# Performance work log

Measured on AMD Instinct MI355X. Metric: run time of the kernel, lower is better.

## Reference

```python
import jax, jax.numpy as jnp
import numpy as np
import math

T = 0.01      # temperature (init kwarg)
CUT = 32      # high-frequency cutoff (init kwarg)


def scalar_field(n, F):
    """Random scalar field of size [n,n] from the first m=F.shape[0] sine modes."""
    m = F.shape[0]
    xs = jnp.linspace(0.0, 1.0, n, dtype=F.dtype)
    k = jnp.arange(1, m + 1, dtype=F.dtype)
    i, j = jnp.meshgrid(k, k, indexing='ij')          # [m,m]
    r = jnp.sqrt(i * i + j * j)
    e = (r < m + 0.5).astype(F.dtype) / r             # sqrt(1/energy) mask
    s = jnp.sin(math.pi * xs[:, None] * k[None, :])   # [n,m]
    c = F * e
    return jnp.einsum('ij,xi,yj->yx', c, s, s)        # [n,n]


def remap_linear(a, dx, dy):
    """Bilinear remap of a [..., n, m] by displacement fields dx, dy of shape [n,m]."""
    n, m = a.shape[-2], a.shape[-1]
    dt = dx.dtype
    yy, xx = jnp.meshgrid(jnp.arange(n, dtype=dt), jnp.arange(m, dtype=dt), indexing='ij')
    xn = jnp.clip(xx + dx, 0, m - 1)
    yn = jnp.clip(yy + dy, 0, n - 1)
    xf = jnp.floor(xn).astype(jnp.int32)
    yf = jnp.floor(yn).astype(jnp.int32)
    xc = jnp.ceil(xn).astype(jnp.int32)
    yc = jnp.ceil(yn).astype(jnp.int32)
    xv = (xn - xf.astype(dt))[None, None]  # [1,1,n,m] broadcast over batch, channel
    yv = (yn - yf.astype(dt))[None, None]
    g = lambda yi, xi: a[..., yi, xi]      # gather corners -> [B,C,n,m]
    return ((1 - yv) * (1 - xv) * g(yf, xf)
            + (1 - yv) * xv * g(yf, xc)
            + yv * (1 - xv) * g(yc, xf)
            + yv * xv * g(yc, xc))


def setup_inputs() -> dict:
    key = jax.random.key(0)
    k1, k2, k3 = jax.random.split(key, 3)
    x = jax.random.normal(k1, (128, 3, 224, 224), dtype=jnp.float32)
    F_x = jax.random.normal(k2, (CUT, CUT), dtype=jnp.float32)
    F_y = jax.random.normal(k3, (CUT, CUT), dtype=jnp.float32)
    return {"x": x, "F_x": F_x, "F_y": F_y}


def reference(x, F_x, F_y):
    n = x.shape[-1]
    u = scalar_field(n, F_x)
    v = scalar_field(n, F_y)
    dx = (T ** 0.5) * u * n
    dy = (T ** 0.5) * v * n
    return remap_linear(x, dx, dy)
```

## Files before the change

kernel.cpp:

```cpp
#include <hip/hip_runtime.h>
#include <hip/hip_fp16.h>

#define N 224
#define M 32
#define NPIX (N * N)
#define NPLANE 384
#define PLT 128
#define NPGRP 3
#define TTILE 4704
#define NPT 6
#define RPX 64
#define NCHUNK (NPIX / RPX)
#define NXCD 8
#define CPX (NCHUNK / NXCD)
#define PI_F 3.14159265358979323846f

typedef float vfloat4 __attribute__((ext_vector_type(4)));
typedef float vfloat2 __attribute__((ext_vector_type(2)));

__global__ __launch_bounds__(256) void fused_field_transpose(
    const float* __restrict__ x, const float* __restrict__ Fx,
    const float* __restrict__ Fy, int4* __restrict__ tab,
    __half* __restrict__ xt)
{
    const int tid = threadIdx.x;

    if (blockIdx.x < N) {
        __shared__ float cx[M][M];
        __shared__ float cy[M][M];
        __shared__ float sy[M];

        const int y = blockIdx.x;

        for (int idx = tid; idx < M * M; idx += 256) {
            const int i = idx / M, j = idx % M;
            const float fi = (float)(i + 1), fj = (float)(j + 1);
            const float r = sqrtf(fi * fi + fj * fj);
            const float e = (r < (float)M + 0.5f) ? (1.0f / r) : 0.0f;
            cx[i][j] = Fx[idx] * e;
            cy[i][j] = Fy[idx] * e;
        }
        if (tid < M) {
            const float ys = (float)y / (float)(N - 1);
            sy[tid] = sinf(PI_F * ys * (float)(tid + 1));
        }
        __syncthreads();

        if (tid >= N) return;
        const int xi = tid;

        float sx[M];
        const float xsv = (float)xi / (float)(N - 1);
#pragma unroll
        for (int i = 0; i < M; ++i)
            sx[i] = sinf(PI_F * xsv * (float)(i + 1));

        float u = 0.0f, v = 0.0f;
#pragma unroll 1
        for (int j = 0; j < M; ++j) {
            float tx = 0.0f, ty = 0.0f;
#pragma unroll
            for (int i = 0; i < M; ++i) {
                tx = fmaf(cx[i][j], sx[i], tx);
                ty = fmaf(cy[i][j], sx[i], ty);
            }
            const float syj = sy[j];
            u = fmaf(syj, tx, u);
            v = fmaf(syj, ty, v);
        }

        const float dxv = 22.4f * u;
        const float dyv = 22.4f * v;
        const float xn = fminf(fmaxf((float)xi + dxv, 0.0f), (float)(N - 1));
        const float yn = fminf(fmaxf((float)y + dyv, 0.0f), (float)(N - 1));
        const int bx = min((int)floorf(xn), N - 2);
        const int by = min((int)floorf(yn), N - 2);
        const float fx = xn - (float)bx;
        const float fy = yn - (float)by;

        tab[y * N + xi] = make_int4(by * N + bx,
                                    __float_as_int(fx), __float_as_int(fy), 0);
        return;
    }

    __shared__ float t[64][65];

    const int tb    = blockIdx.x - N;
    const int ptile = tb % NPT;
    const int xtile = tb / NPT;
    const int pl0   = ptile * 64;
    const int pix0  = xtile * 64;

    const int c = tid & 15;
    const int q = (tid >> 4) & 3;
    const int w = tid >> 6;

#pragma unroll
    for (int i = 0; i < 4; ++i) {
        const int p = w * 16 + i * 4 + q;
        const vfloat4 v = *(const vfloat4*)(
            x + (size_t)(pl0 + p) * NPIX + pix0 + 4 * c);
        t[p][4 * c + 0] = v.x;
        t[p][4 * c + 1] = v.y;
        t[p][4 * c + 2] = v.z;
        t[p][4 * c + 3] = v.w;
    }
    __syncthreads();

    __half* xo = xt + (size_t)pix0 * NPLANE + pl0;
#pragma unroll
    for (int s = 0; s < 4; ++s) {
        const int P = w * 16 + s * 4 + q;
        const float f0 = t[4 * c + 0][P];
        const float f1 = t[4 * c + 1][P];
        const float f2 = t[4 * c + 2][P];
        const float f3 = t[4 * c + 3][P];
        union { uint2 u; __half2 hh[2]; } pk;
        pk.hh[0] = __floats2half2_rn(f0, f1);
        pk.hh[1] = __floats2half2_rn(f2, f3);
        *(uint2*)&xo[(size_t)P * NPLANE + 4 * c] = pk.u;
    }
}

__global__ __launch_bounds__(256) void remap_kernel(
    const __half* __restrict__ xt, const int4* __restrict__ tab,
    float* __restrict__ out)
{
    __shared__ float tile[RPX][130];
    __shared__ int4 ltab[RPX];

    const int tid = threadIdx.x;
    const int w = tid >> 6, l = tid & 63;

    const int bid   = blockIdx.x;
    const int xcd   = bid & 7;
    const int local = bid >> 3;
    const int pg    = local / CPX;
    const int chunk = xcd * CPX + (local % CPX);
    const int pix0  = chunk * RPX;

    if (tid < RPX) ltab[tid] = tab[pix0 + tid];
    __syncthreads();

    const __half2* base = (const __half2*)xt;
    const int pgoff = pg * (PLT / 2);

#pragma unroll 8
    for (int i = 0; i < 16; ++i) {
        const int pl = w * 16 + i;
        const int4 tb = ltab[pl];
        const float fx = __int_as_float(tb.y);
        const float fy = __int_as_float(tb.z);
        const float omx = 1.0f - fx, omy = 1.0f - fy;
        const float w00 = omy * omx, w01 = omy * fx;
        const float w10 = fy * omx,  w11 = fy * fx;

        const size_t b0 = (size_t)tb.x * (NPLANE / 2) + pgoff;
        const float2 c00 = __half22float2(base[b0 + l]);
        const float2 c01 = __half22float2(base[b0 + NPLANE / 2 + l]);
        const float2 c10 = __half22float2(base[b0 + (size_t)N * (NPLANE/2) + l]);
        const float2 c11 = __half22float2(base[b0 + (size_t)(N + 1) * (NPLANE/2) + l]);

        float2 o;
        o.x = w00 * c00.x + w01 * c01.x + w10 * c10.x + w11 * c11.x;
        o.y = w00 * c00.y + w01 * c01.y + w10 * c10.y + w11 * c11.y;
        *(float2*)&tile[pl][2 * l] = o;
    }
    __syncthreads();

    const int l2 = tid & 31, jg = tid >> 5;
    float* ob = out + (size_t)pg * PLT * NPIX + pix0;
#pragma unroll
    for (int s = 0; s < 16; ++s) {
        const int j = jg * 16 + s;
        vfloat2 o2;
        o2.x = tile[2 * l2][j];
        o2.y = tile[2 * l2 + 1][j];
        __builtin_nontemporal_store(o2, (vfloat2*)&ob[(size_t)j * NPIX + 2 * l2]);
    }
}

extern "C" void kernel_launch(void* const* d_in, const int* in_sizes, int n_in,
                              void* d_out, int out_size, void* d_ws, size_t ws_size,
                              hipStream_t stream) {
    const float* x  = (const float*)d_in[0];
    const float* Fx = (const float*)d_in[1];
    const float* Fy = (const float*)d_in[2];
    float* out = (float*)d_out;

    int4* tab = (int4*)d_ws;
    const size_t tab_bytes = (size_t)NPIX * sizeof(int4);
    __half* xt = (__half*)((char*)d_ws + tab_bytes);

    fused_field_transpose<<<N + TTILE, 256, 0, stream>>>(x, Fx, Fy, tab, xt);
    remap_kernel<<<NCHUNK * NPGRP, 256, 0, stream>>>(xt, tab, out);
}
```

Before: 49.59 us.

## Widen transpose tiles to 128 planes with 16-byte half stores and permuted layout

Each transpose block now handles 128 planes by 64 pixels instead of 64 by 64, so there are half as many blocks, and each thread writes 16-byte packed half stores instead of 8-byte ones. The planes are interleaved in a permuted order within each 8-half group, and the remap kernel's shared-tile write index is permuted to match when it unpacks. The field-computation blocks move to the end of the grid and share one pooled shared-memory buffer. The larger shared buffer may reduce occupancy, and correctness depends on the two kernels agreeing on the permuted plane order.

```diff
diff --git a/kernel.cpp b/kernel.cpp
--- a/kernel.cpp
+++ b/kernel.cpp
@@ -7,8 +7,8 @@
 #define NPLANE 384
 #define PLT 128
 #define NPGRP 3
-#define TTILE 4704
-#define NPT 6
+#define NXT 784
+#define TTILE (NXT * NPGRP)
 #define RPX 64
 #define NCHUNK (NPIX / RPX)
 #define NXCD 8
@@ -23,14 +23,15 @@
     const float* __restrict__ Fy, int4* __restrict__ tab,
     __half* __restrict__ xt)
 {
+    __shared__ float pool[128 * 65];
     const int tid = threadIdx.x;
 
-    if (blockIdx.x < N) {
-        __shared__ float cx[M][M];
-        __shared__ float cy[M][M];
-        __shared__ float sy[M];
+    if (blockIdx.x >= TTILE) {
+        float (*cx)[M] = (float(*)[M])pool;
+        float (*cy)[M] = (float(*)[M])(pool + M * M);
+        float *sy = pool + 2 * M * M;
 
-        const int y = blockIdx.x;
+        const int y = blockIdx.x - TTILE;
 
         for (int idx = tid; idx < M * M; idx += 256) {
             const int i = idx / M, j = idx % M;
@@ -83,12 +84,12 @@
         return;
     }
 
-    __shared__ float t[64][65];
+    float (*t)[65] = (float(*)[65])pool;
 
-    const int tb    = blockIdx.x - N;
-    const int ptile = tb % NPT;
-    const int xtile = tb / NPT;
-    const int pl0   = ptile * 64;
+    const int tb    = blockIdx.x;
+    const int pg    = tb / NXT;
+    const int xtile = tb % NXT;
+    const int pl0   = pg * 128;
     const int pix0  = xtile * 64;
 
     const int c = tid & 15;
@@ -96,8 +97,8 @@
     const int w = tid >> 6;
 
 #pragma unroll
-    for (int i = 0; i < 4; ++i) {
-        const int p = w * 16 + i * 4 + q;
+    for (int i = 0; i < 8; ++i) {
+        const int p = 16 * i + (tid >> 4);
         const vfloat4 v = *(const vfloat4*)(
             x + (size_t)(pl0 + p) * NPIX + pix0 + 4 * c);
         t[p][4 * c + 0] = v.x;
@@ -111,14 +112,12 @@
 #pragma unroll
     for (int s = 0; s < 4; ++s) {
         const int P = w * 16 + s * 4 + q;
-        const float f0 = t[4 * c + 0][P];
-        const float f1 = t[4 * c + 1][P];
-        const float f2 = t[4 * c + 2][P];
-        const float f3 = t[4 * c + 3][P];
-        union { uint2 u; __half2 hh[2]; } pk;
-        pk.hh[0] = __floats2half2_rn(f0, f1);
-        pk.hh[1] = __floats2half2_rn(f2, f3);
-        *(uint2*)&xo[(size_t)P * NPLANE + 4 * c] = pk.u;
+        union { uint4 u; __half2 hh[4]; } pk;
+        pk.hh[0] = __floats2half2_rn(t[4 * c + 0][P],  t[4 * c + 1][P]);
+        pk.hh[1] = __floats2half2_rn(t[4 * c + 2][P],  t[4 * c + 3][P]);
+        pk.hh[2] = __floats2half2_rn(t[4 * c + 64][P], t[4 * c + 65][P]);
+        pk.hh[3] = __floats2half2_rn(t[4 * c + 66][P], t[4 * c + 67][P]);
+        *(uint4*)&xo[(size_t)P * NPLANE + 8 * c] = pk.u;
     }
 }
 
@@ -145,6 +144,8 @@
     const __half2* base = (const __half2*)xt;
     const int pgoff = pg * (PLT / 2);
 
+    const int r0 = 4 * (l >> 2) + 2 * (l & 1) + 64 * ((l & 3) >> 1);
+
 #pragma unroll 8
     for (int i = 0; i < 16; ++i) {
         const int pl = w * 16 + i;
@@ -164,7 +165,7 @@
         float2 o;
         o.x = w00 * c00.x + w01 * c01.x + w10 * c10.x + w11 * c11.x;
         o.y = w00 * c00.y + w01 * c01.y + w10 * c10.y + w11 * c11.y;
-        *(float2*)&tile[pl][2 * l] = o;
+        *(float2*)&tile[pl][r0] = o;
     }
     __syncthreads();
 
@@ -192,6 +193,6 @@
     const size_t tab_bytes = (size_t)NPIX * sizeof(int4);
     __half* xt = (__half*)((char*)d_ws + tab_bytes);
 
-    fused_field_transpose<<<N + TTILE, 256, 0, stream>>>(x, Fx, Fy, tab, xt);
+    fused_field_transpose<<<TTILE + N, 256, 0, stream>>>(x, Fx, Fy, tab, xt);
     remap_kernel<<<NCHUNK * NPGRP, 256, 0, stream>>>(xt, tab, out);
 }
```

New measurement: 65.55 us. 1.32x slower.
